# Performance work log

Measured on AMD Instinct MI355X. Metric: run time of the kernel, lower is better.

## Reference

```python
import jax, jax.numpy as jnp
import numpy as np

N_NODES = 50000


def _gcn_conv(x, W, b, src, dst, n_nodes):
    """PyG GCNConv: add self-loops, symmetric normalization, aggregate, linear, bias.
    x: [N, Fin], W: [Fin, Fout], b: [Fout], src/dst: [E] int.
    """
    loop = jnp.arange(n_nodes, dtype=src.dtype)
    src_f = jnp.concatenate([src, loop])  # [E + N]
    dst_f = jnp.concatenate([dst, loop])
    # degree over incoming edges (edge weights are all 1 after self-loops)
    deg = jax.ops.segment_sum(jnp.ones_like(src_f, dtype=x.dtype), dst_f,
                              num_segments=n_nodes)
    dinv = jnp.where(deg > 0, jax.lax.rsqrt(deg), 0.0)
    norm = dinv[src_f] * dinv[dst_f]  # [E + N]
    h = x @ W  # [N, Fout] -- transform before propagate (Fin >= Fout path)
    msg = h[src_f] * norm[:, None]  # gather + per-edge scale
    out = jax.ops.segment_sum(msg, dst_f, num_segments=n_nodes)  # scatter-add
    return out + b


def setup_inputs() -> dict:
    key = jax.random.key(0)
    k_x, k_e, k_w1, k_w2 = jax.random.split(key, 4)
    in_ch, out_ch = 128, 64
    hid = 2 * out_ch
    n_edges = 800000
    x = jax.random.normal(k_x, (N_NODES, in_ch), dtype=jnp.float32)
    edge_index = jax.random.randint(k_e, (2, n_edges), 0, N_NODES, dtype=jnp.int64)
    # Glorot-ish init for weights, zero bias (matches PyG defaults)
    W1 = jax.random.normal(k_w1, (in_ch, hid), dtype=jnp.float32) / np.sqrt(in_ch)
    b1 = jnp.zeros((hid,), dtype=jnp.float32)
    W2 = jax.random.normal(k_w2, (hid, out_ch), dtype=jnp.float32) / np.sqrt(hid)
    b2 = jnp.zeros((out_ch,), dtype=jnp.float32)
    return {"x": x, "edge_index": edge_index, "W1": W1, "b1": b1, "W2": W2, "b2": b2}


def reference(x, edge_index, W1, b1, W2, b2):
    src, dst = edge_index[0], edge_index[1]
    h = jnp.tanh(_gcn_conv(x, W1, b1, src, dst, N_NODES))
    return _gcn_conv(h, W2, b2, src, dst, N_NODES)
```

## Files before the change

### kernel.cpp

```cpp
#include <hip/hip_runtime.h>
#include <stdint.h>

#define N_NODES 50000
#define IN_CH   128
#define HID     128
#define OUT_CH  64

#define CBITS 8
#define NCB   196
#define CAP   8192
#define APB   4096

#define XPAD  136
#define G1BLK 782

typedef unsigned int   uint32;
typedef unsigned short ushort16;
typedef __attribute__((ext_vector_type(8))) short short8;
typedef __attribute__((ext_vector_type(4))) float f32x4;

static __device__ __forceinline__ ushort16 f32_to_bf16(float f) {
    uint32 u = __float_as_uint(f);
    u = (u + 0x7fffu + ((u >> 16) & 1u)) >> 16;
    return (ushort16)u;
}
static __device__ __forceinline__ float bf16lo_to_f32(uint32 u) {
    return __uint_as_float(u << 16);
}
static __device__ __forceinline__ float bf16hi_to_f32(uint32 u) {
    return __uint_as_float(u & 0xffff0000u);
}
#define RLI(v, l) __builtin_amdgcn_readlane((v), (l))
#define RLF(v, l) __uint_as_float((uint32)__builtin_amdgcn_readlane((int)__float_as_uint(v), (l)))

__global__ __launch_bounds__(256) void build1_kernel(
    const int* __restrict__ src, const int* __restrict__ dst,
    int* __restrict__ gcur, uint32* __restrict__ ebuf2, int E, int nA,
    const float* __restrict__ W1, const float* __restrict__ W2,
    ushort16* __restrict__ w1t, ushort16* __restrict__ w2t) {
    __shared__ int hist[256];
    __shared__ int excl[256];
    __shared__ int fcur[256];
    __shared__ int gbase[256];
    __shared__ uint32 obuf[APB];
    const int t = threadIdx.x;

    if ((int)blockIdx.x >= nA) {
        int i = ((int)blockIdx.x - nA) * 256 + t;
        if (i < 128 * 128) {
            int k = i >> 7, n = i & 127;
            w1t[n * 128 + k] = f32_to_bf16(W1[k * 128 + n]);
        }
        if (i < 128 * 64) {
            int k = i >> 6, n = i & 63;
            w2t[n * 128 + k] = f32_to_bf16(W2[k * 64 + n]);
        }
        return;
    }

    const int e0 = blockIdx.x * APB;
    const int nv = min(APB, E - e0);

    hist[t] = 0;
    __syncthreads();

    uint32 u[16];
    #pragma unroll
    for (int j = 0; j < 16; ++j) {
        int i = t + 256 * j;
        u[j] = 0xffffffffu;
        if (i < nv) {
            int e = e0 + i;
            int s = src[e], d = dst[e];
            if ((unsigned)d < N_NODES && (unsigned)s < N_NODES) {
                u[j] = (uint32)s | ((uint32)d << 16);
                atomicAdd(&hist[(unsigned)d >> CBITS], 1);
            }
        }
    }
    __syncthreads();

    excl[t] = hist[t];
    __syncthreads();
    #pragma unroll
    for (int off = 1; off < 256; off <<= 1) {
        int v = (t >= off) ? excl[t - off] : 0;
        __syncthreads();
        excl[t] += v;
        __syncthreads();
    }
    int myexcl = excl[t] - hist[t];
    if (hist[t] > 0) gbase[t] = t * CAP + atomicAdd(&gcur[t], hist[t]);
    __syncthreads();
    excl[t] = myexcl;
    fcur[t] = myexcl;
    __syncthreads();

    #pragma unroll
    for (int j = 0; j < 16; ++j) {
        if (u[j] != 0xffffffffu) {
            int b = u[j] >> (16 + CBITS);
            int pos = atomicAdd(&fcur[b], 1);
            obuf[pos] = u[j];
        }
    }
    __syncthreads();

    for (int i = t; i < nv; i += 256) {
        uint32 v = obuf[i];
        int b = v >> (16 + CBITS);
        int gpos = gbase[b] + (i - excl[b]);
        if (gpos < (b + 1) * CAP) ebuf2[gpos] = v;
    }
}

__global__ __launch_bounds__(256) void build2_kernel(
    const uint32* __restrict__ ebuf2, const int* __restrict__ gcur,
    ushort16* __restrict__ ebuf16, int* __restrict__ offs,
    int* __restrict__ degi, float* __restrict__ dinv,
    const float* __restrict__ x, const ushort16* __restrict__ w1t,
    ushort16* __restrict__ h1b) {
    __shared__ __align__(16) char smem[53248];
    const int t = threadIdx.x;

    if (blockIdx.x >= NCB) {
        ushort16* xs = (ushort16*)smem;
        ushort16* wt = (ushort16*)(smem + 64 * XPAD * 2);
        const int block_row = ((int)blockIdx.x - NCB) * 64;

        {
            const uint4* g = (const uint4*)w1t;
            #pragma unroll
            for (int j = 0; j < 8; ++j) {
                int idx = t + 256 * j;
                int row = idx >> 4, c = idx & 15;
                uint4 v = g[idx];
                *(uint4*)&wt[row * XPAD + c * 8] = v;
            }
        }
        {
            #pragma unroll
            for (int j = 0; j < 8; ++j) {
                int idx = t + 256 * j;
                int row = idx >> 5, c4 = idx & 31;
                int gr = block_row + row; if (gr >= N_NODES) gr = N_NODES - 1;
                float4 v = *(const float4*)(x + (size_t)gr * IN_CH + c4 * 4);
                uint32 p0 = (uint32)f32_to_bf16(v.x) | ((uint32)f32_to_bf16(v.y) << 16);
                uint32 p1 = (uint32)f32_to_bf16(v.z) | ((uint32)f32_to_bf16(v.w) << 16);
                uint32* dp = (uint32*)&xs[row * XPAD + c4 * 4];
                dp[0] = p0; dp[1] = p1;
            }
        }
        __syncthreads();

        const int wv = t >> 6, lane = t & 63;
        const int r16 = lane & 15, kq = lane >> 4;
        f32x4 acc[8];
        #pragma unroll
        for (int n = 0; n < 8; ++n) acc[n] = (f32x4){0.f, 0.f, 0.f, 0.f};

        const ushort16* xrow = &xs[(wv * 16 + r16) * XPAD + kq * 8];
        #pragma unroll
        for (int kk = 0; kk < 4; ++kk) {
            short8 a = *(const short8*)(xrow + kk * 32);
            #pragma unroll
            for (int n = 0; n < 8; ++n) {
                short8 b = *(const short8*)&wt[(n * 16 + r16) * XPAD + kk * 32 + kq * 8];
                acc[n] = __builtin_amdgcn_mfma_f32_16x16x32_bf16(a, b, acc[n], 0, 0, 0);
            }
        }

        #pragma unroll
        for (int n = 0; n < 8; ++n) {
            #pragma unroll
            for (int j = 0; j < 4; ++j) {
                int gr = block_row + wv * 16 + kq * 4 + j;
                if (gr < N_NODES)
                    h1b[(size_t)gr * HID + n * 16 + r16] = f32_to_bf16(acc[n][j]);
            }
        }
        return;
    }

    uint32*   sbuf = (uint32*)smem;
    ushort16* obuf = (ushort16*)(smem + CAP * 4);
    int* fh = (int*)(smem + CAP * 4 + CAP * 2);
    int* fx = fh + 256;
    int* fc = fx + 256;
    int* gs = fc + 256;
    const int b = blockIdx.x;

    {
        int c = (t < NCB) ? min(gcur[t], CAP) : 0;
        gs[t] = c;
        __syncthreads();
        #pragma unroll
        for (int off = 1; off < 256; off <<= 1) {
            int v = (t >= off) ? gs[t - off] : 0;
            __syncthreads();
            gs[t] += v;
            __syncthreads();
        }
    }
    const int nb = min(gcur[b], CAP);
    const int obase = gs[b] - nb;
    __syncthreads();

    fh[t] = 0;
    __syncthreads();
    for (int i = t; i < nb; i += 256) {
        uint32 v = ebuf2[b * CAP + i];
        sbuf[i] = v;
        atomicAdd(&fh[(v >> 16) & 255], 1);
    }
    __syncthreads();

    fx[t] = fh[t];
    __syncthreads();
    #pragma unroll
    for (int off = 1; off < 256; off <<= 1) {
        int v = (t >= off) ? fx[t - off] : 0;
        __syncthreads();
        fx[t] += v;
        __syncthreads();
    }
    int ex = fx[t] - fh[t];
    fc[t] = ex;

    int n = b * 256 + t;
    if (n < N_NODES) {
        degi[n] = fh[t];
        offs[n] = obase + ex;
        dinv[n] = rsqrtf(1.0f + (float)fh[t]);
    }
    __syncthreads();

    for (int i = t; i < nb; i += 256) {
        uint32 v = sbuf[i];
        int nl = (v >> 16) & 255;
        int pos = atomicAdd(&fc[nl], 1);
        obuf[pos] = (ushort16)(v & 0xffffu);
    }
    __syncthreads();
    for (int i = t; i < nb; i += 256) ebuf16[obase + i] = obuf[i];
}

__global__ __launch_bounds__(256) void gather1_kernel(
    const int* __restrict__ offs, const int* __restrict__ degi,
    const ushort16* __restrict__ ebuf16, const float* __restrict__ dinv,
    const ushort16* __restrict__ h1b, const float* __restrict__ b1,
    ushort16* __restrict__ a1b) {
    int node = blockIdx.x * 4 + (threadIdx.x >> 6);
    int lane = threadIdx.x & 63;
    if (node >= N_NODES) return;
    float di = dinv[node];
    int beg = offs[node];
    int cnt = degi[node];

    uint32 us = ((const uint32*)(h1b + (size_t)node * HID))[lane];
    float ax = bf16lo_to_f32(us) * di * di;
    float ay = bf16hi_to_f32(us) * di * di;

    for (int base = 0; base < cnt; base += 64) {
        int m = min(cnt - base, 64);
        int e_l = 0; float w_l = 0.f;
        if (lane < m) {
            e_l = (int)ebuf16[beg + base + lane];
            e_l = min(e_l, N_NODES - 1);
            w_l = dinv[e_l] * di;
        }
        int i = 0;
        for (; i + 8 <= m; i += 8) {
            int s0 = RLI(e_l, i),     s1 = RLI(e_l, i + 1);
            int s2 = RLI(e_l, i + 2), s3 = RLI(e_l, i + 3);
            int s4 = RLI(e_l, i + 4), s5 = RLI(e_l, i + 5);
            int s6 = RLI(e_l, i + 6), s7 = RLI(e_l, i + 7);
            float w0 = RLF(w_l, i),     w1 = RLF(w_l, i + 1);
            float w2 = RLF(w_l, i + 2), w3 = RLF(w_l, i + 3);
            float w4 = RLF(w_l, i + 4), w5 = RLF(w_l, i + 5);
            float w6 = RLF(w_l, i + 6), w7 = RLF(w_l, i + 7);
            uint32 u0 = ((const uint32*)(h1b + (size_t)s0 * HID))[lane];
            uint32 u1 = ((const uint32*)(h1b + (size_t)s1 * HID))[lane];
            uint32 u2 = ((const uint32*)(h1b + (size_t)s2 * HID))[lane];
            uint32 u3 = ((const uint32*)(h1b + (size_t)s3 * HID))[lane];
            uint32 u4 = ((const uint32*)(h1b + (size_t)s4 * HID))[lane];
            uint32 u5 = ((const uint32*)(h1b + (size_t)s5 * HID))[lane];
            uint32 u6 = ((const uint32*)(h1b + (size_t)s6 * HID))[lane];
            uint32 u7 = ((const uint32*)(h1b + (size_t)s7 * HID))[lane];
            ax += bf16lo_to_f32(u0) * w0 + bf16lo_to_f32(u1) * w1
                + bf16lo_to_f32(u2) * w2 + bf16lo_to_f32(u3) * w3
                + bf16lo_to_f32(u4) * w4 + bf16lo_to_f32(u5) * w5
                + bf16lo_to_f32(u6) * w6 + bf16lo_to_f32(u7) * w7;
            ay += bf16hi_to_f32(u0) * w0 + bf16hi_to_f32(u1) * w1
                + bf16hi_to_f32(u2) * w2 + bf16hi_to_f32(u3) * w3
                + bf16hi_to_f32(u4) * w4 + bf16hi_to_f32(u5) * w5
                + bf16hi_to_f32(u6) * w6 + bf16hi_to_f32(u7) * w7;
        }
        for (; i < m; ++i) {
            int s0 = RLI(e_l, i);
            float w0 = RLF(w_l, i);
            uint32 u0 = ((const uint32*)(h1b + (size_t)s0 * HID))[lane];
            ax += bf16lo_to_f32(u0) * w0;
            ay += bf16hi_to_f32(u0) * w0;
        }
    }
    float2 bb = ((const float2*)b1)[lane];
    float tx = tanhf(ax + bb.x);
    float ty = tanhf(ay + bb.y);
    uint32 pk = (uint32)f32_to_bf16(tx) | ((uint32)f32_to_bf16(ty) << 16);
    ((uint32*)(a1b + (size_t)node * HID))[lane] = pk;
}

__global__ __launch_bounds__(256) void gemm2_mfma_kernel(
    const ushort16* __restrict__ a1b, const ushort16* __restrict__ w2t,
    ushort16* __restrict__ h2b) {
    __shared__ __align__(16) ushort16 xs[64 * XPAD];
    __shared__ __align__(16) ushort16 wt[64 * XPAD];
    const int tid = threadIdx.x;
    const int block_row = blockIdx.x * 64;

    {
        const uint4* g = (const uint4*)w2t;
        #pragma unroll
        for (int j = 0; j < 4; ++j) {
            int idx = tid + 256 * j;
            int row = idx >> 4, c = idx & 15;
            uint4 v = g[idx];
            *(uint4*)&wt[row * XPAD + c * 8] = v;
        }
    }
    {
        #pragma unroll
        for (int j = 0; j < 4; ++j) {
            int idx = tid + 256 * j;
            int row = idx >> 4, c = idx & 15;
            int gr = block_row + row; if (gr >= N_NODES) gr = N_NODES - 1;
            uint4 v = *(const uint4*)(a1b + (size_t)gr * HID + c * 8);
            *(uint4*)&xs[row * XPAD + c * 8] = v;
        }
    }
    __syncthreads();

    const int wv = tid >> 6, lane = tid & 63;
    const int r16 = lane & 15, kq = lane >> 4;
    f32x4 acc[4];
    #pragma unroll
    for (int n = 0; n < 4; ++n) acc[n] = (f32x4){0.f, 0.f, 0.f, 0.f};

    const ushort16* xrow = &xs[(wv * 16 + r16) * XPAD + kq * 8];
    #pragma unroll
    for (int kk = 0; kk < 4; ++kk) {
        short8 a = *(const short8*)(xrow + kk * 32);
        #pragma unroll
        for (int n = 0; n < 4; ++n) {
            short8 b = *(const short8*)&wt[(n * 16 + r16) * XPAD + kk * 32 + kq * 8];
            acc[n] = __builtin_amdgcn_mfma_f32_16x16x32_bf16(a, b, acc[n], 0, 0, 0);
        }
    }

    #pragma unroll
    for (int n = 0; n < 4; ++n) {
        #pragma unroll
        for (int j = 0; j < 4; ++j) {
            int gr = block_row + wv * 16 + kq * 4 + j;
            if (gr < N_NODES)
                h2b[(size_t)gr * OUT_CH + n * 16 + r16] = f32_to_bf16(acc[n][j]);
        }
    }
}

__global__ __launch_bounds__(256) void gather2_kernel(
    const int* __restrict__ offs, const int* __restrict__ degi,
    const ushort16* __restrict__ ebuf16, const float* __restrict__ dinv,
    const ushort16* __restrict__ h2b, const float* __restrict__ b2,
    float* __restrict__ out) {
    int node = blockIdx.x * 4 + (threadIdx.x >> 6);
    int lane = threadIdx.x & 63;
    if (node >= N_NODES) return;
    float di = dinv[node];
    int beg = offs[node];
    int cnt = degi[node];

    float self = __uint_as_float(((uint32)h2b[(size_t)node * OUT_CH + lane]) << 16);
    float acc = b2[lane] + self * di * di;

    for (int base = 0; base < cnt; base += 64) {
        int m = min(cnt - base, 64);
        int e_l = 0; float w_l = 0.f;
        if (lane < m) {
            e_l = (int)ebuf16[beg + base + lane];
            e_l = min(e_l, N_NODES - 1);
            w_l = dinv[e_l] * di;
        }
        int i = 0;
        for (; i + 8 <= m; i += 8) {
            int s0 = RLI(e_l, i),     s1 = RLI(e_l, i + 1);
            int s2 = RLI(e_l, i + 2), s3 = RLI(e_l, i + 3);
            int s4 = RLI(e_l, i + 4), s5 = RLI(e_l, i + 5);
            int s6 = RLI(e_l, i + 6), s7 = RLI(e_l, i + 7);
            float w0 = RLF(w_l, i),     w1 = RLF(w_l, i + 1);
            float w2 = RLF(w_l, i + 2), w3 = RLF(w_l, i + 3);
            float w4 = RLF(w_l, i + 4), w5 = RLF(w_l, i + 5);
            float w6 = RLF(w_l, i + 6), w7 = RLF(w_l, i + 7);
            float v0 = __uint_as_float(((uint32)h2b[(size_t)s0 * OUT_CH + lane]) << 16);
            float v1 = __uint_as_float(((uint32)h2b[(size_t)s1 * OUT_CH + lane]) << 16);
            float v2 = __uint_as_float(((uint32)h2b[(size_t)s2 * OUT_CH + lane]) << 16);
            float v3 = __uint_as_float(((uint32)h2b[(size_t)s3 * OUT_CH + lane]) << 16);
            float v4 = __uint_as_float(((uint32)h2b[(size_t)s4 * OUT_CH + lane]) << 16);
            float v5 = __uint_as_float(((uint32)h2b[(size_t)s5 * OUT_CH + lane]) << 16);
            float v6 = __uint_as_float(((uint32)h2b[(size_t)s6 * OUT_CH + lane]) << 16);
            float v7 = __uint_as_float(((uint32)h2b[(size_t)s7 * OUT_CH + lane]) << 16);
            acc += v0 * w0 + v1 * w1 + v2 * w2 + v3 * w3
                 + v4 * w4 + v5 * w5 + v6 * w6 + v7 * w7;
        }
        for (; i < m; ++i) {
            int s0 = RLI(e_l, i);
            float w0 = RLF(w_l, i);
            float v0 = __uint_as_float(((uint32)h2b[(size_t)s0 * OUT_CH + lane]) << 16);
            acc += v0 * w0;
        }
    }
    out[(size_t)node * OUT_CH + lane] = acc;
}

extern "C" void kernel_launch(void* const* d_in, const int* in_sizes, int n_in,
                              void* d_out, int out_size, void* d_ws, size_t ws_size,
                              hipStream_t stream) {
    const float* x  = (const float*)d_in[0];
    const int*   ei = (const int*)d_in[1];
    const float* W1 = (const float*)d_in[2];
    const float* b1 = (const float*)d_in[3];
    const float* W2 = (const float*)d_in[4];
    const float* b2 = (const float*)d_in[5];
    float* out = (float*)d_out;

    const int E = in_sizes[1] / 2;
    const int* src = ei;
    const int* dst = ei + E;
    const int nA = (E + APB - 1) / APB;

    float* dinv   = (float*)d_ws;
    int* degi     = (int*)(dinv + N_NODES);
    int* offs     = degi + N_NODES;
    int* gcur     = offs + N_NODES;
    ushort16* w1t = (ushort16*)(gcur + NCB);
    ushort16* w2t = w1t + 128 * 128;
    ushort16* ebuf16 = w2t + 64 * 128;
    uintptr_t p   = (uintptr_t)(ebuf16 + (size_t)NCB * CAP);
    p = (p + 15) & ~(uintptr_t)15;
    ushort16* a1b = (ushort16*)p;
    uint32* ebuf2 = (uint32*)a1b;
    ushort16* h1b = a1b + (size_t)N_NODES * HID;
    ushort16* h2b = h1b + (size_t)N_NODES * HID;

    hipMemsetAsync(gcur, 0, NCB * sizeof(int), stream);
    build1_kernel<<<nA + 64, 256, 0, stream>>>(src, dst, gcur, ebuf2, E, nA,
                                               W1, W2, w1t, w2t);
    build2_kernel<<<NCB + G1BLK, 256, 0, stream>>>(ebuf2, gcur, ebuf16, offs, degi, dinv,
                                                   x, w1t, h1b);
    gather1_kernel<<<(N_NODES + 3) / 4, 256, 0, stream>>>(offs, degi, ebuf16, dinv, h1b, b1, a1b);
    gemm2_mfma_kernel<<<G1BLK, 256, 0, stream>>>(a1b, w2t, h2b);
    gather2_kernel<<<(N_NODES + 3) / 4, 256, 0, stream>>>(offs, degi, ebuf16, dinv, h2b, b2, out);
}
```

Measured before the change: 113.3 us.

## Fuse layer-1 gather/tanh with layer-2 MFMA GEMM via shared-memory tile

Merges the first-layer neighbor aggregation (with bias and tanh) and the second-layer bf16 MFMA GEMM into one kernel. Each 256-thread block aggregates 64 nodes, one wave handling 16 nodes in turn, and writes the tanh activations straight into an LDS tile that then feeds the MFMA. This removes the global a1b intermediate round trip and one kernel launch. In exchange the grid shrinks from 12500 to 782 blocks, so each wave gathers its nodes serially with fewer waves to hide latency, and W2 fragments are now read from global memory instead of being staged in LDS.

New measurement: 136.5 us. +20.5%, slower.

```diff
diff --git a/kernel.cpp b/kernel.cpp
--- a/kernel.cpp
+++ b/kernel.cpp
@@ -245,115 +245,92 @@
     for (int i = t; i < nb; i += 256) ebuf16[obase + i] = obuf[i];
 }
 
-__global__ __launch_bounds__(256) void gather1_kernel(
+__global__ __launch_bounds__(256) void fused_mid_kernel(
     const int* __restrict__ offs, const int* __restrict__ degi,
     const ushort16* __restrict__ ebuf16, const float* __restrict__ dinv,
     const ushort16* __restrict__ h1b, const float* __restrict__ b1,
-    ushort16* __restrict__ a1b) {
-    int node = blockIdx.x * 4 + (threadIdx.x >> 6);
-    int lane = threadIdx.x & 63;
-    if (node >= N_NODES) return;
-    float di = dinv[node];
-    int beg = offs[node];
-    int cnt = degi[node];
-
-    uint32 us = ((const uint32*)(h1b + (size_t)node * HID))[lane];
-    float ax = bf16lo_to_f32(us) * di * di;
-    float ay = bf16hi_to_f32(us) * di * di;
-
-    for (int base = 0; base < cnt; base += 64) {
-        int m = min(cnt - base, 64);
-        int e_l = 0; float w_l = 0.f;
-        if (lane < m) {
-            e_l = (int)ebuf16[beg + base + lane];
-            e_l = min(e_l, N_NODES - 1);
-            w_l = dinv[e_l] * di;
-        }
-        int i = 0;
-        for (; i + 8 <= m; i += 8) {
-            int s0 = RLI(e_l, i),     s1 = RLI(e_l, i + 1);
-            int s2 = RLI(e_l, i + 2), s3 = RLI(e_l, i + 3);
-            int s4 = RLI(e_l, i + 4), s5 = RLI(e_l, i + 5);
-            int s6 = RLI(e_l, i + 6), s7 = RLI(e_l, i + 7);
-            float w0 = RLF(w_l, i),     w1 = RLF(w_l, i + 1);
-            float w2 = RLF(w_l, i + 2), w3 = RLF(w_l, i + 3);
-            float w4 = RLF(w_l, i + 4), w5 = RLF(w_l, i + 5);
-            float w6 = RLF(w_l, i + 6), w7 = RLF(w_l, i + 7);
-            uint32 u0 = ((const uint32*)(h1b + (size_t)s0 * HID))[lane];
-            uint32 u1 = ((const uint32*)(h1b + (size_t)s1 * HID))[lane];
-            uint32 u2 = ((const uint32*)(h1b + (size_t)s2 * HID))[lane];
-            uint32 u3 = ((const uint32*)(h1b + (size_t)s3 * HID))[lane];
-            uint32 u4 = ((const uint32*)(h1b + (size_t)s4 * HID))[lane];
-            uint32 u5 = ((const uint32*)(h1b + (size_t)s5 * HID))[lane];
-            uint32 u6 = ((const uint32*)(h1b + (size_t)s6 * HID))[lane];
-            uint32 u7 = ((const uint32*)(h1b + (size_t)s7 * HID))[lane];
-            ax += bf16lo_to_f32(u0) * w0 + bf16lo_to_f32(u1) * w1
-                + bf16lo_to_f32(u2) * w2 + bf16lo_to_f32(u3) * w3
-                + bf16lo_to_f32(u4) * w4 + bf16lo_to_f32(u5) * w5
-                + bf16lo_to_f32(u6) * w6 + bf16lo_to_f32(u7) * w7;
-            ay += bf16hi_to_f32(u0) * w0 + bf16hi_to_f32(u1) * w1
-                + bf16hi_to_f32(u2) * w2 + bf16hi_to_f32(u3) * w3
-                + bf16hi_to_f32(u4) * w4 + bf16hi_to_f32(u5) * w5
-                + bf16hi_to_f32(u6) * w6 + bf16hi_to_f32(u7) * w7;
-        }
-        for (; i < m; ++i) {
-            int s0 = RLI(e_l, i);
-            float w0 = RLF(w_l, i);
-            uint32 u0 = ((const uint32*)(h1b + (size_t)s0 * HID))[lane];
-            ax += bf16lo_to_f32(u0) * w0;
-            ay += bf16hi_to_f32(u0) * w0;
-        }
-    }
+    const ushort16* __restrict__ w2t, ushort16* __restrict__ h2b) {
+    __shared__ __align__(16) ushort16 a1[64 * XPAD];
+    const int t = threadIdx.x;
+    const int wv = t >> 6, lane = t & 63;
+    const int block_row = blockIdx.x * 64;
+
     float2 bb = ((const float2*)b1)[lane];
-    float tx = tanhf(ax + bb.x);
-    float ty = tanhf(ay + bb.y);
-    uint32 pk = (uint32)f32_to_bf16(tx) | ((uint32)f32_to_bf16(ty) << 16);
-    ((uint32*)(a1b + (size_t)node * HID))[lane] = pk;
-}
-
-__global__ __launch_bounds__(256) void gemm2_mfma_kernel(
-    const ushort16* __restrict__ a1b, const ushort16* __restrict__ w2t,
-    ushort16* __restrict__ h2b) {
-    __shared__ __align__(16) ushort16 xs[64 * XPAD];
-    __shared__ __align__(16) ushort16 wt[64 * XPAD];
-    const int tid = threadIdx.x;
-    const int block_row = blockIdx.x * 64;
-
-    {
-        const uint4* g = (const uint4*)w2t;
-        #pragma unroll
-        for (int j = 0; j < 4; ++j) {
-            int idx = tid + 256 * j;
-            int row = idx >> 4, c = idx & 15;
-            uint4 v = g[idx];
-            *(uint4*)&wt[row * XPAD + c * 8] = v;
-        }
-    }
-    {
-        #pragma unroll
-        for (int j = 0; j < 4; ++j) {
-            int idx = tid + 256 * j;
-            int row = idx >> 4, c = idx & 15;
-            int gr = block_row + row; if (gr >= N_NODES) gr = N_NODES - 1;
-            uint4 v = *(const uint4*)(a1b + (size_t)gr * HID + c * 8);
-            *(uint4*)&xs[row * XPAD + c * 8] = v;
-        }
-    }
-    __syncthreads();
-
-    const int wv = tid >> 6, lane = tid & 63;
+
+    for (int it = 0; it < 16; ++it) {
+        int lrow = wv * 16 + it;
+        int node = block_row + lrow;
+        if (node >= N_NODES) node = N_NODES - 1;
+        float di = dinv[node];
+        int beg = offs[node];
+        int cnt = degi[node];
+
+        uint32 us = ((const uint32*)(h1b + (size_t)node * HID))[lane];
+        float ax = bf16lo_to_f32(us) * di * di;
+        float ay = bf16hi_to_f32(us) * di * di;
+
+        for (int base = 0; base < cnt; base += 64) {
+            int m = min(cnt - base, 64);
+            int e_l = 0; float w_l = 0.f;
+            if (lane < m) {
+                e_l = (int)ebuf16[beg + base + lane];
+                e_l = min(e_l, N_NODES - 1);
+                w_l = dinv[e_l] * di;
+            }
+            int i = 0;
+            for (; i + 8 <= m; i += 8) {
+                int s0 = RLI(e_l, i),     s1 = RLI(e_l, i + 1);
+                int s2 = RLI(e_l, i + 2), s3 = RLI(e_l, i + 3);
+                int s4 = RLI(e_l, i + 4), s5 = RLI(e_l, i + 5);
+                int s6 = RLI(e_l, i + 6), s7 = RLI(e_l, i + 7);
+                float w0 = RLF(w_l, i),     float_w1 = RLF(w_l, i + 1);
+                float w2 = RLF(w_l, i + 2), w3 = RLF(w_l, i + 3);
+                float w4 = RLF(w_l, i + 4), w5 = RLF(w_l, i + 5);
+                float w6 = RLF(w_l, i + 6), w7 = RLF(w_l, i + 7);
+                uint32 u0 = ((const uint32*)(h1b + (size_t)s0 * HID))[lane];
+                uint32 u1 = ((const uint32*)(h1b + (size_t)s1 * HID))[lane];
+                uint32 u2 = ((const uint32*)(h1b + (size_t)s2 * HID))[lane];
+                uint32 u3 = ((const uint32*)(h1b + (size_t)s3 * HID))[lane];
+                uint32 u4 = ((const uint32*)(h1b + (size_t)s4 * HID))[lane];
+                uint32 u5 = ((const uint32*)(h1b + (size_t)s5 * HID))[lane];
+                uint32 u6 = ((const uint32*)(h1b + (size_t)s6 * HID))[lane];
+                uint32 u7 = ((const uint32*)(h1b + (size_t)s7 * HID))[lane];
+                ax += bf16lo_to_f32(u0) * w0 + bf16lo_to_f32(u1) * float_w1
+                    + bf16lo_to_f32(u2) * w2 + bf16lo_to_f32(u3) * w3
+                    + bf16lo_to_f32(u4) * w4 + bf16lo_to_f32(u5) * w5
+                    + bf16lo_to_f32(u6) * w6 + bf16lo_to_f32(u7) * w7;
+                ay += bf16hi_to_f32(u0) * w0 + bf16hi_to_f32(u1) * float_w1
+                    + bf16hi_to_f32(u2) * w2 + bf16hi_to_f32(u3) * w3
+                    + bf16hi_to_f32(u4) * w4 + bf16hi_to_f32(u5) * w5
+                    + bf16hi_to_f32(u6) * w6 + bf16hi_to_f32(u7) * w7;
+            }
+            for (; i < m; ++i) {
+                int s0 = RLI(e_l, i);
+                float w0 = RLF(w_l, i);
+                uint32 u0 = ((const uint32*)(h1b + (size_t)s0 * HID))[lane];
+                ax += bf16lo_to_f32(u0) * w0;
+                ay += bf16hi_to_f32(u0) * w0;
+            }
+        }
+        float tx = tanhf(ax + bb.x);
+        float ty = tanhf(ay + bb.y);
+        uint32 pk = (uint32)f32_to_bf16(tx) | ((uint32)f32_to_bf16(ty) << 16);
+        *(uint32*)&a1[lrow * XPAD + 2 * lane] = pk;
+    }
+    __syncthreads();
+
     const int r16 = lane & 15, kq = lane >> 4;
     f32x4 acc[4];
     #pragma unroll
     for (int n = 0; n < 4; ++n) acc[n] = (f32x4){0.f, 0.f, 0.f, 0.f};
 
-    const ushort16* xrow = &xs[(wv * 16 + r16) * XPAD + kq * 8];
+    const ushort16* xrow = &a1[(wv * 16 + r16) * XPAD + kq * 8];
     #pragma unroll
     for (int kk = 0; kk < 4; ++kk) {
         short8 a = *(const short8*)(xrow + kk * 32);
         #pragma unroll
         for (int n = 0; n < 4; ++n) {
-            short8 b = *(const short8*)&wt[(n * 16 + r16) * XPAD + kk * 32 + kq * 8];
+            short8 b = *(const short8*)&w2t[(n * 16 + r16) * 128 + kk * 32 + kq * 8];
             acc[n] = __builtin_amdgcn_mfma_f32_16x16x32_bf16(a, b, acc[n], 0, 0, 0);
         }
     }
@@ -448,9 +425,8 @@
     ushort16* ebuf16 = w2t + 64 * 128;
     uintptr_t p   = (uintptr_t)(ebuf16 + (size_t)NCB * CAP);
     p = (p + 15) & ~(uintptr_t)15;
-    ushort16* a1b = (ushort16*)p;
-    uint32* ebuf2 = (uint32*)a1b;
-    ushort16* h1b = a1b + (size_t)N_NODES * HID;
+    uint32* ebuf2 = (uint32*)p;
+    ushort16* h1b = (ushort16*)(ebuf2 + (size_t)NCB * CAP);
     ushort16* h2b = h1b + (size_t)N_NODES * HID;
 
     hipMemsetAsync(gcur, 0, NCB * sizeof(int), stream);
@@ -458,7 +434,6 @@
                                                W1, W2, w1t, w2t);
     build2_kernel<<<NCB + G1BLK, 256, 0, stream>>>(ebuf2, gcur, ebuf16, offs, degi, dinv,
                                                    x, w1t, h1b);
-    gather1_kernel<<<(N_NODES + 3) / 4, 256, 0, stream>>>(offs, degi, ebuf16, dinv, h1b, b1, a1b);
-    gemm2_mfma_kernel<<<G1BLK, 256, 0, stream>>>(a1b, w2t, h2b);
+    fused_mid_kernel<<<G1BLK, 256, 0, stream>>>(offs, degi, ebuf16, dinv, h1b, b1, w2t, h2b);
     gather2_kernel<<<(N_NODES + 3) / 4, 256, 0, stream>>>(offs, degi, ebuf16, dinv, h2b, b2, out);
 }
```

## Split gather feature columns across blocks and process four edges per wave

Applied to the files above, without the earlier changes.

Both aggregation kernels now split each node's feature row into 16-lane column groups, with the group chosen by block index. Each wavefront's four quarter-waves handle different edges at the same time, using shuffles to broadcast edge index and weight, then combine partial sums with xor-shuffles. The goal is more independent memory requests in flight per wave, and 4-byte loads instead of 2-byte loads in the second gather. In exchange, the grid is several times larger, edge lists and dinv are re-read once per column group, and readlane is replaced by the costlier bpermute-based shuffles.

New measurement: 171.9 us. 51.7% more time.

```diff
diff --git a/kernel.cpp b/kernel.cpp
--- a/kernel.cpp
+++ b/kernel.cpp
@@ -30,8 +30,6 @@
 static __device__ __forceinline__ float bf16hi_to_f32(uint32 u) {
     return __uint_as_float(u & 0xffff0000u);
 }
-#define RLI(v, l) __builtin_amdgcn_readlane((v), (l))
-#define RLF(v, l) __uint_as_float((uint32)__builtin_amdgcn_readlane((int)__float_as_uint(v), (l)))
 
 __global__ __launch_bounds__(256) void build1_kernel(
     const int* __restrict__ src, const int* __restrict__ dst,
@@ -250,16 +248,17 @@
     const ushort16* __restrict__ ebuf16, const float* __restrict__ dinv,
     const ushort16* __restrict__ h1b, const float* __restrict__ b1,
     ushort16* __restrict__ a1b) {
-    int node = blockIdx.x * 4 + (threadIdx.x >> 6);
-    int lane = threadIdx.x & 63;
+    const int g    = blockIdx.x & 3;
+    const int node = (blockIdx.x >> 2) * 4 + (threadIdx.x >> 6);
+    const int lane = threadIdx.x & 63;
+    const int q = lane >> 4, c16 = lane & 15;
     if (node >= N_NODES) return;
     float di = dinv[node];
     int beg = offs[node];
     int cnt = degi[node];
 
-    uint32 us = ((const uint32*)(h1b + (size_t)node * HID))[lane];
-    float ax = bf16lo_to_f32(us) * di * di;
-    float ay = bf16hi_to_f32(us) * di * di;
+    const uint32* hcol = (const uint32*)h1b + g * 16 + c16;
+    float ax = 0.f, ay = 0.f;
 
     for (int base = 0; base < cnt; base += 64) {
         int m = min(cnt - base, 64);
@@ -269,46 +268,32 @@
             e_l = min(e_l, N_NODES - 1);
             w_l = dinv[e_l] * di;
         }
-        int i = 0;
-        for (; i + 8 <= m; i += 8) {
-            int s0 = RLI(e_l, i),     s1 = RLI(e_l, i + 1);
-            int s2 = RLI(e_l, i + 2), s3 = RLI(e_l, i + 3);
-            int s4 = RLI(e_l, i + 4), s5 = RLI(e_l, i + 5);
-            int s6 = RLI(e_l, i + 6), s7 = RLI(e_l, i + 7);
-            float w0 = RLF(w_l, i),     w1 = RLF(w_l, i + 1);
-            float w2 = RLF(w_l, i + 2), w3 = RLF(w_l, i + 3);
-            float w4 = RLF(w_l, i + 4), w5 = RLF(w_l, i + 5);
-            float w6 = RLF(w_l, i + 6), w7 = RLF(w_l, i + 7);
-            uint32 u0 = ((const uint32*)(h1b + (size_t)s0 * HID))[lane];
-            uint32 u1 = ((const uint32*)(h1b + (size_t)s1 * HID))[lane];
-            uint32 u2 = ((const uint32*)(h1b + (size_t)s2 * HID))[lane];
-            uint32 u3 = ((const uint32*)(h1b + (size_t)s3 * HID))[lane];
-            uint32 u4 = ((const uint32*)(h1b + (size_t)s4 * HID))[lane];
-            uint32 u5 = ((const uint32*)(h1b + (size_t)s5 * HID))[lane];
-            uint32 u6 = ((const uint32*)(h1b + (size_t)s6 * HID))[lane];
-            uint32 u7 = ((const uint32*)(h1b + (size_t)s7 * HID))[lane];
-            ax += bf16lo_to_f32(u0) * w0 + bf16lo_to_f32(u1) * w1
-                + bf16lo_to_f32(u2) * w2 + bf16lo_to_f32(u3) * w3
-                + bf16lo_to_f32(u4) * w4 + bf16lo_to_f32(u5) * w5
-                + bf16lo_to_f32(u6) * w6 + bf16lo_to_f32(u7) * w7;
-            ay += bf16hi_to_f32(u0) * w0 + bf16hi_to_f32(u1) * w1
-                + bf16hi_to_f32(u2) * w2 + bf16hi_to_f32(u3) * w3
-                + bf16hi_to_f32(u4) * w4 + bf16hi_to_f32(u5) * w5
-                + bf16hi_to_f32(u6) * w6 + bf16hi_to_f32(u7) * w7;
-        }
-        for (; i < m; ++i) {
-            int s0 = RLI(e_l, i);
-            float w0 = RLF(w_l, i);
-            uint32 u0 = ((const uint32*)(h1b + (size_t)s0 * HID))[lane];
-            ax += bf16lo_to_f32(u0) * w0;
-            ay += bf16hi_to_f32(u0) * w0;
-        }
-    }
-    float2 bb = ((const float2*)b1)[lane];
-    float tx = tanhf(ax + bb.x);
-    float ty = tanhf(ay + bb.y);
-    uint32 pk = (uint32)f32_to_bf16(tx) | ((uint32)f32_to_bf16(ty) << 16);
-    ((uint32*)(a1b + (size_t)node * HID))[lane] = pk;
+        for (int i = 0; i < m; i += 16) {
+            #pragma unroll
+            for (int k = 0; k < 4; ++k) {
+                int idx = i + 4 * k + q;
+                int s   = __shfl(e_l, idx);
+                float w = __shfl(w_l, idx);
+                uint32 u = hcol[(size_t)s * 64];
+                ax += bf16lo_to_f32(u) * w;
+                ay += bf16hi_to_f32(u) * w;
+            }
+        }
+    }
+    ax += __shfl_xor(ax, 16); ax += __shfl_xor(ax, 32);
+    ay += __shfl_xor(ay, 16); ay += __shfl_xor(ay, 32);
+
+    uint32 us = hcol[(size_t)node * 64];
+    ax += bf16lo_to_f32(us) * di * di;
+    ay += bf16hi_to_f32(us) * di * di;
+
+    if (q == 0) {
+        float2 bb = ((const float2*)b1)[g * 16 + c16];
+        float tx = tanhf(ax + bb.x);
+        float ty = tanhf(ay + bb.y);
+        uint32 pk = (uint32)f32_to_bf16(tx) | ((uint32)f32_to_bf16(ty) << 16);
+        ((uint32*)a1b)[(size_t)node * 64 + g * 16 + c16] = pk;
+    }
 }
 
 __global__ __launch_bounds__(256) void gemm2_mfma_kernel(
@@ -374,15 +359,17 @@
     const ushort16* __restrict__ ebuf16, const float* __restrict__ dinv,
     const ushort16* __restrict__ h2b, const float* __restrict__ b2,
     float* __restrict__ out) {
-    int node = blockIdx.x * 4 + (threadIdx.x >> 6);
-    int lane = threadIdx.x & 63;
+    const int g    = blockIdx.x & 1;
+    const int node = (blockIdx.x >> 1) * 4 + (threadIdx.x >> 6);
+    const int lane = threadIdx.x & 63;
+    const int q = lane >> 4, c16 = lane & 15;
     if (node >= N_NODES) return;
     float di = dinv[node];
     int beg = offs[node];
     int cnt = degi[node];
 
-    float self = __uint_as_float(((uint32)h2b[(size_t)node * OUT_CH + lane]) << 16);
-    float acc = b2[lane] + self * di * di;
+    const uint32* hcol = (const uint32*)h2b + g * 16 + c16;
+    float ax = 0.f, ay = 0.f;
 
     for (int base = 0; base < cnt; base += 64) {
         int m = min(cnt - base, 64);
@@ -392,35 +379,30 @@
             e_l = min(e_l, N_NODES - 1);
             w_l = dinv[e_l] * di;
         }
-        int i = 0;
-        for (; i + 8 <= m; i += 8) {
-            int s0 = RLI(e_l, i),     s1 = RLI(e_l, i + 1);
-            int s2 = RLI(e_l, i + 2), s3 = RLI(e_l, i + 3);
-            int s4 = RLI(e_l, i + 4), s5 = RLI(e_l, i + 5);
-            int s6 = RLI(e_l, i + 6), s7 = RLI(e_l, i + 7);
-            float w0 = RLF(w_l, i),     w1 = RLF(w_l, i + 1);
-            float w2 = RLF(w_l, i + 2), w3 = RLF(w_l, i + 3);
-            float w4 = RLF(w_l, i + 4), w5 = RLF(w_l, i + 5);
-            float w6 = RLF(w_l, i + 6), w7 = RLF(w_l, i + 7);
-            float v0 = __uint_as_float(((uint32)h2b[(size_t)s0 * OUT_CH + lane]) << 16);
-            float v1 = __uint_as_float(((uint32)h2b[(size_t)s1 * OUT_CH + lane]) << 16);
-            float v2 = __uint_as_float(((uint32)h2b[(size_t)s2 * OUT_CH + lane]) << 16);
-            float v3 = __uint_as_float(((uint32)h2b[(size_t)s3 * OUT_CH + lane]) << 16);
-            float v4 = __uint_as_float(((uint32)h2b[(size_t)s4 * OUT_CH + lane]) << 16);
-            float v5 = __uint_as_float(((uint32)h2b[(size_t)s5 * OUT_CH + lane]) << 16);
-            float v6 = __uint_as_float(((uint32)h2b[(size_t)s6 * OUT_CH + lane]) << 16);
-            float v7 = __uint_as_float(((uint32)h2b[(size_t)s7 * OUT_CH + lane]) << 16);
-            acc += v0 * w0 + v1 * w1 + v2 * w2 + v3 * w3
-                 + v4 * w4 + v5 * w5 + v6 * w6 + v7 * w7;
-        }
-        for (; i < m; ++i) {
-            int s0 = RLI(e_l, i);
-            float w0 = RLF(w_l, i);
-            float v0 = __uint_as_float(((uint32)h2b[(size_t)s0 * OUT_CH + lane]) << 16);
-            acc += v0 * w0;
-        }
-    }
-    out[(size_t)node * OUT_CH + lane] = acc;
+        for (int i = 0; i < m; i += 16) {
+            #pragma unroll
+            for (int k = 0; k < 4; ++k) {
+                int idx = i + 4 * k + q;
+                int s   = __shfl(e_l, idx);
+                float w = __shfl(w_l, idx);
+                uint32 u = hcol[(size_t)s * 32];
+                ax += bf16lo_to_f32(u) * w;
+                ay += bf16hi_to_f32(u) * w;
+            }
+        }
+    }
+    ax += __shfl_xor(ax, 16); ax += __shfl_xor(ax, 32);
+    ay += __shfl_xor(ay, 16); ay += __shfl_xor(ay, 32);
+
+    uint32 us = hcol[(size_t)node * 32];
+    ax += bf16lo_to_f32(us) * di * di;
+    ay += bf16hi_to_f32(us) * di * di;
+
+    if (q == 0) {
+        float2 bb = ((const float2*)b2)[g * 16 + c16];
+        float2 r; r.x = ax + bb.x; r.y = ay + bb.y;
+        ((float2*)out)[(size_t)node * 32 + g * 16 + c16] = r;
+    }
 }
 
 extern "C" void kernel_launch(void* const* d_in, const int* in_sizes, int n_in,
@@ -458,7 +440,7 @@
                                                W1, W2, w1t, w2t);
     build2_kernel<<<NCB + G1BLK, 256, 0, stream>>>(ebuf2, gcur, ebuf16, offs, degi, dinv,
                                                    x, w1t, h1b);
-    gather1_kernel<<<(N_NODES + 3) / 4, 256, 0, stream>>>(offs, degi, ebuf16, dinv, h1b, b1, a1b);
+    gather1_kernel<<<(N_NODES / 4) * 4, 256, 0, stream>>>(offs, degi, ebuf16, dinv, h1b, b1, a1b);
     gemm2_mfma_kernel<<<G1BLK, 256, 0, stream>>>(a1b, w2t, h2b);
-    gather2_kernel<<<(N_NODES + 3) / 4, 256, 0, stream>>>(offs, degi, ebuf16, dinv, h2b, b2, out);
-}
+    gather2_kernel<<<(N_NODES / 4) * 2, 256, 0, stream>>>(offs, degi, ebuf16, dinv, h2b, b2, out);
+}
```

## Move GEMM1 into build1 launch and fold memset into weight-prep kernel

Applied to the files above, without the earlier changes.

The hipMemsetAsync of the bucket counters is replaced by a small prep kernel that also converts and transposes the weights to bf16. The first MFMA GEMM (x·W1) moves from build2 into build1, so it runs concurrently with the edge bucketing pass rather than with the per-bucket sort. build2 then runs only its NCB sort blocks. This rebalances work across the kernels and drops a memset, but adds a separate prep launch and makes build1 depend on the converted weights being ready.

New measurement: 113.6 us. About the same (+0.3%).

```diff
diff --git a/kernel.cpp b/kernel.cpp
--- a/kernel.cpp
+++ b/kernel.cpp
@@ -33,100 +33,38 @@
 #define RLI(v, l) __builtin_amdgcn_readlane((v), (l))
 #define RLF(v, l) __uint_as_float((uint32)__builtin_amdgcn_readlane((int)__float_as_uint(v), (l)))
 
+__global__ __launch_bounds__(256) void prep_kernel(
+    const float* __restrict__ W1, const float* __restrict__ W2,
+    ushort16* __restrict__ w1t, ushort16* __restrict__ w2t,
+    int* __restrict__ gcur) {
+    const int t = threadIdx.x;
+    if (blockIdx.x == 64) {
+        if (t < NCB) gcur[t] = 0;
+        return;
+    }
+    int i = blockIdx.x * 256 + t;
+    if (i < 128 * 128) {
+        int k = i >> 7, n = i & 127;
+        w1t[n * 128 + k] = f32_to_bf16(W1[k * 128 + n]);
+    }
+    if (i < 128 * 64) {
+        int k = i >> 6, n = i & 63;
+        w2t[n * 128 + k] = f32_to_bf16(W2[k * 64 + n]);
+    }
+}
+
 __global__ __launch_bounds__(256) void build1_kernel(
     const int* __restrict__ src, const int* __restrict__ dst,
     int* __restrict__ gcur, uint32* __restrict__ ebuf2, int E, int nA,
-    const float* __restrict__ W1, const float* __restrict__ W2,
-    ushort16* __restrict__ w1t, ushort16* __restrict__ w2t) {
-    __shared__ int hist[256];
-    __shared__ int excl[256];
-    __shared__ int fcur[256];
-    __shared__ int gbase[256];
-    __shared__ uint32 obuf[APB];
-    const int t = threadIdx.x;
-
-    if ((int)blockIdx.x >= nA) {
-        int i = ((int)blockIdx.x - nA) * 256 + t;
-        if (i < 128 * 128) {
-            int k = i >> 7, n = i & 127;
-            w1t[n * 128 + k] = f32_to_bf16(W1[k * 128 + n]);
-        }
-        if (i < 128 * 64) {
-            int k = i >> 6, n = i & 63;
-            w2t[n * 128 + k] = f32_to_bf16(W2[k * 64 + n]);
-        }
-        return;
-    }
-
-    const int e0 = blockIdx.x * APB;
-    const int nv = min(APB, E - e0);
-
-    hist[t] = 0;
-    __syncthreads();
-
-    uint32 u[16];
-    #pragma unroll
-    for (int j = 0; j < 16; ++j) {
-        int i = t + 256 * j;
-        u[j] = 0xffffffffu;
-        if (i < nv) {
-            int e = e0 + i;
-            int s = src[e], d = dst[e];
-            if ((unsigned)d < N_NODES && (unsigned)s < N_NODES) {
-                u[j] = (uint32)s | ((uint32)d << 16);
-                atomicAdd(&hist[(unsigned)d >> CBITS], 1);
-            }
-        }
-    }
-    __syncthreads();
-
-    excl[t] = hist[t];
-    __syncthreads();
-    #pragma unroll
-    for (int off = 1; off < 256; off <<= 1) {
-        int v = (t >= off) ? excl[t - off] : 0;
-        __syncthreads();
-        excl[t] += v;
-        __syncthreads();
-    }
-    int myexcl = excl[t] - hist[t];
-    if (hist[t] > 0) gbase[t] = t * CAP + atomicAdd(&gcur[t], hist[t]);
-    __syncthreads();
-    excl[t] = myexcl;
-    fcur[t] = myexcl;
-    __syncthreads();
-
-    #pragma unroll
-    for (int j = 0; j < 16; ++j) {
-        if (u[j] != 0xffffffffu) {
-            int b = u[j] >> (16 + CBITS);
-            int pos = atomicAdd(&fcur[b], 1);
-            obuf[pos] = u[j];
-        }
-    }
-    __syncthreads();
-
-    for (int i = t; i < nv; i += 256) {
-        uint32 v = obuf[i];
-        int b = v >> (16 + CBITS);
-        int gpos = gbase[b] + (i - excl[b]);
-        if (gpos < (b + 1) * CAP) ebuf2[gpos] = v;
-    }
-}
-
-__global__ __launch_bounds__(256) void build2_kernel(
-    const uint32* __restrict__ ebuf2, const int* __restrict__ gcur,
-    ushort16* __restrict__ ebuf16, int* __restrict__ offs,
-    int* __restrict__ degi, float* __restrict__ dinv,
     const float* __restrict__ x, const ushort16* __restrict__ w1t,
     ushort16* __restrict__ h1b) {
-    __shared__ __align__(16) char smem[53248];
+    __shared__ __align__(16) char smem[52224];
     const int t = threadIdx.x;
 
-    if (blockIdx.x >= NCB) {
+    if ((int)blockIdx.x >= nA) {
         ushort16* xs = (ushort16*)smem;
         ushort16* wt = (ushort16*)(smem + 64 * XPAD * 2);
-        const int block_row = ((int)blockIdx.x - NCB) * 64;
+        const int block_row = ((int)blockIdx.x - nA) * 64;
 
         {
             const uint4* g = (const uint4*)w1t;
@@ -182,13 +120,82 @@
         return;
     }
 
+    int* hist = (int*)smem;
+    int* excl = hist + 256;
+    int* fcur = excl + 256;
+    int* gbase = fcur + 256;
+    uint32* obuf = (uint32*)(gbase + 256);
+
+    const int e0 = blockIdx.x * APB;
+    const int nv = min(APB, E - e0);
+
+    hist[t] = 0;
+    __syncthreads();
+
+    uint32 u[16];
+    #pragma unroll
+    for (int j = 0; j < 16; ++j) {
+        int i = t + 256 * j;
+        u[j] = 0xffffffffu;
+        if (i < nv) {
+            int e = e0 + i;
+            int s = src[e], d = dst[e];
+            if ((unsigned)d < N_NODES && (unsigned)s < N_NODES) {
+                u[j] = (uint32)s | ((uint32)d << 16);
+                atomicAdd(&hist[(unsigned)d >> CBITS], 1);
+            }
+        }
+    }
+    __syncthreads();
+
+    excl[t] = hist[t];
+    __syncthreads();
+    #pragma unroll
+    for (int off = 1; off < 256; off <<= 1) {
+        int v = (t >= off) ? excl[t - off] : 0;
+        __syncthreads();
+        excl[t] += v;
+        __syncthreads();
+    }
+    int myexcl = excl[t] - hist[t];
+    int gb = 0;
+    if (hist[t] > 0) gb = t * CAP + atomicAdd(&gcur[t], hist[t]);
+    __syncthreads();
+    excl[t] = myexcl;
+    fcur[t] = myexcl;
+    gbase[t] = gb;
+    __syncthreads();
+
+    #pragma unroll
+    for (int j = 0; j < 16; ++j) {
+        if (u[j] != 0xffffffffu) {
+            int b = u[j] >> (16 + CBITS);
+            int pos = atomicAdd(&fcur[b], 1);
+            obuf[pos] = u[j];
+        }
+    }
+    __syncthreads();
+
+    for (int i = t; i < nv; i += 256) {
+        uint32 v = obuf[i];
+        int b = v >> (16 + CBITS);
+        int gpos = gbase[b] + (i - excl[b]);
+        if (gpos < (b + 1) * CAP) ebuf2[gpos] = v;
+    }
+}
+
+__global__ __launch_bounds__(256) void build2_kernel(
+    const uint32* __restrict__ ebuf2, const int* __restrict__ gcur,
+    ushort16* __restrict__ ebuf16, int* __restrict__ offs,
+    int* __restrict__ degi, float* __restrict__ dinv) {
+    __shared__ __align__(16) char smem[53248];
     uint32*   sbuf = (uint32*)smem;
     ushort16* obuf = (ushort16*)(smem + CAP * 4);
     int* fh = (int*)(smem + CAP * 4 + CAP * 2);
     int* fx = fh + 256;
     int* fc = fx + 256;
     int* gs = fc + 256;
-    const int b = blockIdx.x;
+    const int b = blockIdx.x, t = threadIdx.x;
 
     {
         int c = (t < NCB) ? min(gcur[t], CAP) : 0;
@@ -453,11 +460,10 @@
     ushort16* h1b = a1b + (size_t)N_NODES * HID;
     ushort16* h2b = h1b + (size_t)N_NODES * HID;
 
-    hipMemsetAsync(gcur, 0, NCB * sizeof(int), stream);
-    build1_kernel<<<nA + 64, 256, 0, stream>>>(src, dst, gcur, ebuf2, E, nA,
-                                               W1, W2, w1t, w2t);
-    build2_kernel<<<NCB + G1BLK, 256, 0, stream>>>(ebuf2, gcur, ebuf16, offs, degi, dinv,
-                                                   x, w1t, h1b);
+    prep_kernel<<<65, 256, 0, stream>>>(W1, W2, w1t, w2t, gcur);
+    build1_kernel<<<nA + G1BLK, 256, 0, stream>>>(src, dst, gcur, ebuf2, E, nA,
+                                                  x, w1t, h1b);
+    build2_kernel<<<NCB, 256, 0, stream>>>(ebuf2, gcur, ebuf16, offs, degi, dinv);
     gather1_kernel<<<(N_NODES + 3) / 4, 256, 0, stream>>>(offs, degi, ebuf16, dinv, h1b, b1, a1b);
     gemm2_mfma_kernel<<<G1BLK, 256, 0, stream>>>(a1b, w2t, h2b);
     gather2_kernel<<<(N_NODES + 3) / 4, 256, 0, stream>>>(offs, degi, ebuf16, dinv, h2b, b2, out);
```
